# Performance work log

Hardware: AMD Instinct MI355X
Metric: run time of the kernel (lower is better)

## Reference

```python
import jax, jax.numpy as jnp
import numpy as np

B, N, E, C = 1, 100000, 1600000, 128


def setup_inputs() -> dict:
    key = jax.random.key(0)
    k1, k2, k3, k4 = jax.random.split(key, 4)
    x = jax.random.normal(k1, (B, N, C), dtype=jnp.float32)
    edge_index = jax.random.randint(k2, (2, E), 0, N, dtype=jnp.int32)
    W_2 = jax.random.normal(k3, (C,), dtype=jnp.float32)
    W_3 = jax.random.normal(k4, (C,), dtype=jnp.float32)
    return {"x": x, "edge_index": edge_index, "W_2": W_2, "W_3": W_3}


def reference(x, edge_index, W_2, W_3):
    # x: [B, N, C]; edge_index: [2, E] (src, dst)
    src, dst = edge_index[0], edge_index[1]
    num_nodes = x.shape[1]
    # per-edge attention weight: w[b,e] = <(x*W_3)[b,src_e], x[b,dst_e]>
    x3 = (x * W_3)[:, src, :]          # [B, E, C] gather
    x4 = x[:, dst, :]                  # [B, E, C] gather
    w = jnp.einsum('bec,bec->be', x3, x4)  # [B, E]
    # value messages with diagonal W_2 scaling, scattered to destination nodes.
    # Equivalent to out = einsum('bij,bih->bjh', dense_adj(w), x*W_2),
    # where dense_adj[src,dst] = w (to_dense_adj sums duplicate edges; so does segment_sum).
    x2 = x * W_2                       # [B, N, C]
    msg = w[..., None] * x2[:, src, :]  # [B, E, C]
    out = jax.vmap(lambda m: jax.ops.segment_sum(m, dst, num_segments=num_nodes))(msg)
    return out  # [B, N, C]
```

## Files before the change

### kernel.cpp

```cpp
#include <hip/hip_runtime.h>
#include <hip/hip_fp16.h>


#define CCH 128
#define BSHIFT 5
#define BWIDTH 32
#define MAXBIN 4096
#define CH 8192
#define LDSCAP 1280
#define TBINS 16
#define NBLKCAP 256


__global__ __launch_bounds__(256) void k_pack_hist(
    const float* __restrict__ x, __half* __restrict__ xh, int n4, int nPack,
    const int* __restrict__ dst, int E, int NBIN, int* __restrict__ hist_bm)
{
    __shared__ int cnt[MAXBIN];
    const int tid = threadIdx.x;

    if (blockIdx.x < nPack) {
        const int i = blockIdx.x * 256 + tid;
        if (i < n4) {
            float4 v = reinterpret_cast<const float4*>(x)[i];
            __half2* o = reinterpret_cast<__half2*>(xh) + (size_t)i * 2;
            o[0] = __floats2half2_rn(v.x, v.y);
            o[1] = __floats2half2_rn(v.z, v.w);
        }
        return;
    }

    const int blk = blockIdx.x - nPack;
    for (int b = tid; b < NBIN; b += 256) cnt[b] = 0;
    __syncthreads();

    const int e0 = blk * CH;
    #pragma unroll
    for (int k = 0; k < CH / 1024; ++k) {
        const int g = (e0 >> 2) + k * 256 + tid;
        const int e = g << 2;
        if (e >= E) continue;
        if (e + 4 <= E) {
            const int4 d4 = reinterpret_cast<const int4*>(dst)[g];
            atomicAdd(&cnt[d4.x >> BSHIFT], 1);
            atomicAdd(&cnt[d4.y >> BSHIFT], 1);
            atomicAdd(&cnt[d4.z >> BSHIFT], 1);
            atomicAdd(&cnt[d4.w >> BSHIFT], 1);
        } else {
            for (int ee = e; ee < E; ++ee) atomicAdd(&cnt[dst[ee] >> BSHIFT], 1);
        }
    }
    __syncthreads();
    int* hb = hist_bm + (size_t)blk * NBIN;
    for (int b = tid; b < NBIN; b += 256) hb[b] = cnt[b];
}


__global__ __launch_bounds__(256) void k_pscan(
    const int* __restrict__ hist_bm, int NBIN, int NBLK, int E_unused,
    int* __restrict__ scanned, unsigned int* __restrict__ status)
{
    __shared__ int tile[TBINS][NBLKCAP + 1];
    __shared__ int sdata[256];
    __shared__ int sbase;
    const int t = threadIdx.x;
    const int B0 = blockIdx.x * TBINS;

    for (int g = t; g < TBINS * (NBLKCAP + 1); g += 256)
        (&tile[0][0])[g] = 0;
    __syncthreads();

    for (int g = t; g < NBLK * TBINS; g += 256) {
        const int blk = g >> 4;
        const int tb  = g & (TBINS - 1);
        const int bin = B0 + tb;
        if (bin < NBIN) tile[tb][blk] = hist_bm[(size_t)blk * NBIN + bin];
    }
    __syncthreads();

    const int tb  = t >> 4;
    const int bk0 = (t & 15) * 16;
    int v[16];
    int local = 0;
    #pragma unroll
    for (int k = 0; k < 16; ++k) { v[k] = tile[tb][bk0 + k]; local += v[k]; }

    sdata[t] = local;
    __syncthreads();
    #pragma unroll
    for (int off = 1; off < 256; off <<= 1) {
        int val = (t >= off) ? sdata[t - off] : 0;
        __syncthreads();
        sdata[t] += val;
        __syncthreads();
    }
    const int incl = sdata[t];
    const int total = sdata[255];

    if (t == 0) {
        __hip_atomic_store(&status[blockIdx.x], (1u << 30) | (unsigned)total,
                           __ATOMIC_RELAXED, __HIP_MEMORY_SCOPE_AGENT);
        int base = 0;
        for (int j = (int)blockIdx.x - 1; j >= 0; --j) {
            unsigned w;
            do {
                w = __hip_atomic_load(&status[j], __ATOMIC_RELAXED,
                                      __HIP_MEMORY_SCOPE_AGENT);
            } while ((w >> 30) == 0u);
            base += (int)(w & 0x3FFFFFFFu);
            if ((w >> 30) == 2u) break;
        }
        __hip_atomic_store(&status[blockIdx.x],
                           (2u << 30) | (unsigned)(base + total),
                           __ATOMIC_RELAXED, __HIP_MEMORY_SCOPE_AGENT);
        sbase = base;
    }
    __syncthreads();

    int run = sbase + (incl - local);
    const int bin = B0 + tb;
    if (bin < NBIN) {
        #pragma unroll
        for (int k = 0; k < 16; ++k) {
            const int blk = bk0 + k;
            if (blk < NBLK) scanned[(size_t)bin * NBLK + blk] = run;
            run += v[k];
        }
    }
}


__global__ __launch_bounds__(256) void k_place(
    const int* __restrict__ src, const int* __restrict__ dst, int E, int NBIN, int NBLK,
    const int* __restrict__ scanned, unsigned int* __restrict__ coarse)
{
    __shared__ int lcur[MAXBIN];
    const int blk = blockIdx.x;
    const int tid = threadIdx.x;
    for (int b = tid; b < NBIN; b += 256)
        lcur[b] = scanned[(size_t)b * NBLK + blk];
    __syncthreads();

    const int e0 = blk * CH;
    #pragma unroll
    for (int k = 0; k < CH / 1024; ++k) {
        const int g = (e0 >> 2) + k * 256 + tid;
        const int e = g << 2;
        if (e >= E) continue;
        if (e + 4 <= E) {
            const int4 d4 = reinterpret_cast<const int4*>(dst)[g];
            const int4 s4 = reinterpret_cast<const int4*>(src)[g];
            int p;
            p = atomicAdd(&lcur[d4.x >> BSHIFT], 1);
            coarse[p] = (unsigned)s4.x | ((unsigned)(d4.x & (BWIDTH - 1)) << 17);
            p = atomicAdd(&lcur[d4.y >> BSHIFT], 1);
            coarse[p] = (unsigned)s4.y | ((unsigned)(d4.y & (BWIDTH - 1)) << 17);
            p = atomicAdd(&lcur[d4.z >> BSHIFT], 1);
            coarse[p] = (unsigned)s4.z | ((unsigned)(d4.z & (BWIDTH - 1)) << 17);
            p = atomicAdd(&lcur[d4.w >> BSHIFT], 1);
            coarse[p] = (unsigned)s4.w | ((unsigned)(d4.w & (BWIDTH - 1)) << 17);
        } else {
            for (int ee = e; ee < E; ++ee) {
                const int d = dst[ee], s = src[ee];
                int p = atomicAdd(&lcur[d >> BSHIFT], 1);
                coarse[p] = (unsigned)s | ((unsigned)(d & (BWIDTH - 1)) << 17);
            }
        }
    }
}


__global__ __launch_bounds__(256) void k_sort_accum(
    const __half* __restrict__ xh,
    const float* __restrict__ W2,
    const float* __restrict__ W3,
    const unsigned int* __restrict__ coarse,
    const int* __restrict__ scanned,
    int NBIN, int NBLK, int E, int N,
    float* __restrict__ out)
{
    __shared__ unsigned int raw[LDSCAP];
    __shared__ int srcl[LDSCAP];
    __shared__ int cnt[BWIDTH], offs[BWIDTH], cur[BWIDTH];

    const int bin  = blockIdx.x;
    const int tid  = threadIdx.x;
    const int lane = tid & 63;
    const int grp  = lane >> 4;
    const int sl   = lane & 15;
    const int gid  = (tid >> 6) * 4 + grp;
    const int choff = sl << 4;
    const char* xb = (const char*)xh;

    union H { int4 i4; __half2 h[4]; };

    const int node0 = (bin << BSHIFT) + gid * 2;
    const int node1 = node0 + 1;
    H uD0, uD1;
    uD0.i4 = make_int4(0, 0, 0, 0);
    uD1.i4 = make_int4(0, 0, 0, 0);
    if (node0 < N) uD0.i4 = *reinterpret_cast<const int4*>(xb + (((size_t)node0) << 8) + choff);
    if (node1 < N) uD1.i4 = *reinterpret_cast<const int4*>(xb + (((size_t)node1) << 8) + choff);

    const size_t i0 = (size_t)bin * NBLK;
    const int beg = scanned[i0];
    const int end = (bin + 1 < NBIN) ? scanned[i0 + NBLK] : E;
    const int mtot = end - beg;
    const int m = (mtot < LDSCAP) ? mtot : LDSCAP;

    if (tid < BWIDTH) cnt[tid] = 0;
    __syncthreads();

    for (int i = tid; i < m; i += 256) {
        unsigned u = coarse[beg + i];
        raw[i] = u;
        atomicAdd(&cnt[u >> 17], 1);
    }
    __syncthreads();

    if (tid < BWIDTH) {
        int c = cnt[tid];
        int v = c;
        #pragma unroll
        for (int d2 = 1; d2 < BWIDTH; d2 <<= 1) {
            int t2 = __shfl_up(v, d2, 64);
            if (tid >= d2) v += t2;
        }
        offs[tid] = v - c;
        cur[tid]  = v - c;
    }
    __syncthreads();

    for (int i = tid; i < m; i += 256) {
        const unsigned u = raw[i];
        const int p = atomicAdd(&cur[u >> 17], 1);
        srcl[p] = (int)(u & 0x1FFFFu);
    }
    __syncthreads();

    const float4 w3a = *reinterpret_cast<const float4*>(W3 + sl * 8);
    const float4 w3b = *reinterpret_cast<const float4*>(W3 + sl * 8 + 4);
    const float4 w2a = *reinterpret_cast<const float4*>(W2 + sl * 8);
    const float4 w2b = *reinterpret_cast<const float4*>(W2 + sl * 8 + 4);

    #pragma unroll
    for (int i = 0; i < 2; ++i) {
        const int node = (i == 0) ? node0 : node1;
        if (node >= N) continue;
        const int dl = gid * 2 + i;
        const H uD = (i == 0) ? uD0 : uD1;

        const float2 e0 = __half22float2(uD.h[0]);
        const float2 e1 = __half22float2(uD.h[1]);
        const float2 e2 = __half22float2(uD.h[2]);
        const float2 e3 = __half22float2(uD.h[3]);
        const float4 va = make_float4(w3a.x * e0.x, w3a.y * e0.y,
                                      w3a.z * e1.x, w3a.w * e1.y);
        const float4 vb = make_float4(w3b.x * e2.x, w3b.y * e2.y,
                                      w3b.z * e3.x, w3b.w * e3.y);

        float4 accA = make_float4(0.f, 0.f, 0.f, 0.f);
        float4 accB = make_float4(0.f, 0.f, 0.f, 0.f);

        const int b0 = offs[dl];
        const int c  = cnt[dl];

        int j = 0;
        for (; j + 4 <= c; j += 4) {
            const int s0 = srcl[b0 + j];
            const int s1 = srcl[b0 + j + 1];
            const int s2 = srcl[b0 + j + 2];
            const int s3 = srcl[b0 + j + 3];
            H u0, u1, u2, u3;
            u0.i4 = *reinterpret_cast<const int4*>(xb + (((size_t)s0) << 8) + choff);
            u1.i4 = *reinterpret_cast<const int4*>(xb + (((size_t)s1) << 8) + choff);
            u2.i4 = *reinterpret_cast<const int4*>(xb + (((size_t)s2) << 8) + choff);
            u3.i4 = *reinterpret_cast<const int4*>(xb + (((size_t)s3) << 8) + choff);
            const float2 f00 = __half22float2(u0.h[0]);
            const float2 f01 = __half22float2(u0.h[1]);
            const float2 f02 = __half22float2(u0.h[2]);
            const float2 f03 = __half22float2(u0.h[3]);
            const float2 f10 = __half22float2(u1.h[0]);
            const float2 f11 = __half22float2(u1.h[1]);
            const float2 f12 = __half22float2(u1.h[2]);
            const float2 f13 = __half22float2(u1.h[3]);
            const float2 f20 = __half22float2(u2.h[0]);
            const float2 f21 = __half22float2(u2.h[1]);
            const float2 f22 = __half22float2(u2.h[2]);
            const float2 f23 = __half22float2(u2.h[3]);
            const float2 f30 = __half22float2(u3.h[0]);
            const float2 f31 = __half22float2(u3.h[1]);
            const float2 f32 = __half22float2(u3.h[2]);
            const float2 f33 = __half22float2(u3.h[3]);
            float p0 = f00.x * va.x + f00.y * va.y + f01.x * va.z + f01.y * va.w
                     + f02.x * vb.x + f02.y * vb.y + f03.x * vb.z + f03.y * vb.w;
            float p1 = f10.x * va.x + f10.y * va.y + f11.x * va.z + f11.y * va.w
                     + f12.x * vb.x + f12.y * vb.y + f13.x * vb.z + f13.y * vb.w;
            float p2 = f20.x * va.x + f20.y * va.y + f21.x * va.z + f21.y * va.w
                     + f22.x * vb.x + f22.y * vb.y + f23.x * vb.z + f23.y * vb.w;
            float p3 = f30.x * va.x + f30.y * va.y + f31.x * va.z + f31.y * va.w
                     + f32.x * vb.x + f32.y * vb.y + f33.x * vb.z + f33.y * vb.w;
            #pragma unroll
            for (int off = 1; off < 16; off <<= 1) {
                p0 += __shfl_xor(p0, off, 64);
                p1 += __shfl_xor(p1, off, 64);
                p2 += __shfl_xor(p2, off, 64);
                p3 += __shfl_xor(p3, off, 64);
            }
            accA.x += p0 * f00.x + p1 * f10.x + p2 * f20.x + p3 * f30.x;
            accA.y += p0 * f00.y + p1 * f10.y + p2 * f20.y + p3 * f30.y;
            accA.z += p0 * f01.x + p1 * f11.x + p2 * f21.x + p3 * f31.x;
            accA.w += p0 * f01.y + p1 * f11.y + p2 * f21.y + p3 * f31.y;
            accB.x += p0 * f02.x + p1 * f12.x + p2 * f22.x + p3 * f32.x;
            accB.y += p0 * f02.y + p1 * f12.y + p2 * f22.y + p3 * f32.y;
            accB.z += p0 * f03.x + p1 * f13.x + p2 * f23.x + p3 * f33.x;
            accB.w += p0 * f03.y + p1 * f13.y + p2 * f23.y + p3 * f33.y;
        }
        for (; j < c; ++j) {
            H u0;
            u0.i4 = *reinterpret_cast<const int4*>(
                xb + (((size_t)srcl[b0 + j]) << 8) + choff);
            const float2 f0 = __half22float2(u0.h[0]);
            const float2 f1 = __half22float2(u0.h[1]);
            const float2 f2 = __half22float2(u0.h[2]);
            const float2 f3 = __half22float2(u0.h[3]);
            float p = f0.x * va.x + f0.y * va.y + f1.x * va.z + f1.y * va.w
                    + f2.x * vb.x + f2.y * vb.y + f3.x * vb.z + f3.y * vb.w;
            #pragma unroll
            for (int off = 1; off < 16; off <<= 1) p += __shfl_xor(p, off, 64);
            accA.x += p * f0.x; accA.y += p * f0.y;
            accA.z += p * f1.x; accA.w += p * f1.y;
            accB.x += p * f2.x; accB.y += p * f2.y;
            accB.z += p * f3.x; accB.w += p * f3.y;
        }
        for (int i2 = LDSCAP; i2 < mtot; ++i2) {
            const unsigned u = coarse[beg + i2];
            if ((int)(u >> 17) != dl) continue;
            H u0;
            u0.i4 = *reinterpret_cast<const int4*>(
                xb + (((size_t)(u & 0x1FFFFu)) << 8) + choff);
            const float2 f0 = __half22float2(u0.h[0]);
            const float2 f1 = __half22float2(u0.h[1]);
            const float2 f2 = __half22float2(u0.h[2]);
            const float2 f3 = __half22float2(u0.h[3]);
            float p = f0.x * va.x + f0.y * va.y + f1.x * va.z + f1.y * va.w
                    + f2.x * vb.x + f2.y * vb.y + f3.x * vb.z + f3.y * vb.w;
            #pragma unroll
            for (int off = 1; off < 16; off <<= 1) p += __shfl_xor(p, off, 64);
            accA.x += p * f0.x; accA.y += p * f0.y;
            accA.z += p * f1.x; accA.w += p * f1.y;
            accB.x += p * f2.x; accB.y += p * f2.y;
            accB.z += p * f3.x; accB.w += p * f3.y;
        }

        accA.x *= w2a.x; accA.y *= w2a.y; accA.z *= w2a.z; accA.w *= w2a.w;
        accB.x *= w2b.x; accB.y *= w2b.y; accB.z *= w2b.z; accB.w *= w2b.w;
        float* orow = out + (size_t)node * CCH + sl * 8;
        *reinterpret_cast<float4*>(orow)     = accA;
        *reinterpret_cast<float4*>(orow + 4) = accB;
    }
}


__global__ __launch_bounds__(256) void edge_gather_scatter(
    const float* __restrict__ x, const int* __restrict__ edge_index,
    const float* __restrict__ W2, const float* __restrict__ W3,
    float* __restrict__ out, int E)
{
    const int e    = (blockIdx.x * blockDim.x + threadIdx.x) >> 6;
    const int lane = threadIdx.x & 63;
    if (e >= E) return;
    const int s = edge_index[e];
    const int d = edge_index[E + e];
    const float2 xs = *reinterpret_cast<const float2*>(x + (size_t)s * CCH + lane * 2);
    const float2 xd = *reinterpret_cast<const float2*>(x + (size_t)d * CCH + lane * 2);
    const float2 w3 = *reinterpret_cast<const float2*>(W3 + lane * 2);
    const float2 w2 = *reinterpret_cast<const float2*>(W2 + lane * 2);
    float p = xs.x * w3.x * xd.x + xs.y * w3.y * xd.y;
    #pragma unroll
    for (int off = 32; off > 0; off >>= 1) p += __shfl_xor(p, off, 64);
    float* o = out + (size_t)d * CCH + lane * 2;
    atomicAdd(o,     p * xs.x * w2.x);
    atomicAdd(o + 1, p * xs.y * w2.y);
}


extern "C" void kernel_launch(void* const* d_in, const int* in_sizes, int n_in,
                              void* d_out, int out_size, void* d_ws, size_t ws_size,
                              hipStream_t stream) {
    const float* x          = (const float*)d_in[0];
    const int*   edge_index = (const int*)  d_in[1];
    const float* W2         = (const float*)d_in[2];
    const float* W3         = (const float*)d_in[3];
    float*       out        = (float*)d_out;

    const int E = in_sizes[1] / 2;
    const int N = out_size / CCH;
    const int* src = edge_index;
    const int* dst = edge_index + E;

    const int NBIN = (N + BWIDTH - 1) >> BSHIFT;
    const int NBLK = (E + CH - 1) / CH;
    const long long Mll = (long long)NBIN * NBLK;
    const int M = (int)Mll;
    const int nb1 = (NBIN + TBINS - 1) / TBINS;

    const size_t xh_bytes = (size_t)N * CCH * 2;
    const size_t need = xh_bytes + (size_t)E * 4 + 2 * (size_t)M * 4 + 4096;

    const bool aligned16 = (((uintptr_t)src & 15) == 0) && (((uintptr_t)dst & 15) == 0);

    if (N <= (1 << 17) && NBIN <= MAXBIN && NBLK <= NBLKCAP && Mll <= (1LL << 20) &&
        nb1 <= 1024 && aligned16 && ws_size >= need) {
        char* base = (char*)d_ws;
        __half* xh        = (__half*)base;       base += xh_bytes;
        unsigned* coarse  = (unsigned*)base;     base += (size_t)E * 4;
        int* hist_bm      = (int*)base;          base += (size_t)M * 4;
        int* scanned      = (int*)base;          base += (size_t)M * 4;
        unsigned* status  = (unsigned*)base;

        const int n4 = N * CCH / 4;
        const int nPack = (n4 + 255) / 256;

        hipMemsetAsync(status, 0, 1024 * sizeof(unsigned), stream);
        k_pack_hist<<<nPack + NBLK, 256, 0, stream>>>(x, xh, n4, nPack,
                                                      dst, E, NBIN, hist_bm);
        k_pscan<<<nb1, 256, 0, stream>>>(hist_bm, NBIN, NBLK, E, scanned, status);
        k_place<<<NBLK, 256, 0, stream>>>(src, dst, E, NBIN, NBLK, scanned, coarse);
        k_sort_accum<<<NBIN, 256, 0, stream>>>(xh, W2, W3, coarse, scanned,
                                               NBIN, NBLK, E, N, out);
        return;
    }

    hipMemsetAsync(d_out, 0, (size_t)out_size * sizeof(float), stream);
    const int grid = (E * 64 + 255) / 256;
    edge_gather_scatter<<<grid, 256, 0, stream>>>(x, edge_index, W2, W3, out, E);
}
```

Measured before the change: 139.3 us.

## Replace decoupled-lookback scan with two-pass scan and move fp16 pack into place kernel

The single-pass decoupled-lookback prefix scan, which needed a status memset and serial spinning, becomes a two-pass scan: per-tile partial sums, then a tiny single-block scan of the tile totals. Consumers now add the tile offset when they read. The x-to-fp16 pack moves from the histogram kernel into the placement kernel, so the short histogram pass runs alone and the pack overlaps with placement. This adds one kernel launch, removes the memset and the serial lookback chain, and adds an extra blocksum load per bin in consumers.

New measurement: 126.9 us. -8.9%, faster.

```diff
diff --git a/kernel.cpp b/kernel.cpp
--- a/kernel.cpp
+++ b/kernel.cpp
@@ -12,25 +12,12 @@
 #define NBLKCAP 256
 
 
-__global__ __launch_bounds__(256) void k_pack_hist(
-    const float* __restrict__ x, __half* __restrict__ xh, int n4, int nPack,
+__global__ __launch_bounds__(256) void k_hist(
     const int* __restrict__ dst, int E, int NBIN, int* __restrict__ hist_bm)
 {
     __shared__ int cnt[MAXBIN];
+    const int blk = blockIdx.x;
     const int tid = threadIdx.x;
-
-    if (blockIdx.x < nPack) {
-        const int i = blockIdx.x * 256 + tid;
-        if (i < n4) {
-            float4 v = reinterpret_cast<const float4*>(x)[i];
-            __half2* o = reinterpret_cast<__half2*>(xh) + (size_t)i * 2;
-            o[0] = __floats2half2_rn(v.x, v.y);
-            o[1] = __floats2half2_rn(v.z, v.w);
-        }
-        return;
-    }
-
-    const int blk = blockIdx.x - nPack;
     for (int b = tid; b < NBIN; b += 256) cnt[b] = 0;
     __syncthreads();
 
@@ -56,13 +43,12 @@
 }
 
 
-__global__ __launch_bounds__(256) void k_pscan(
-    const int* __restrict__ hist_bm, int NBIN, int NBLK, int E_unused,
-    int* __restrict__ scanned, unsigned int* __restrict__ status)
+__global__ __launch_bounds__(256) void k_pscan1(
+    const int* __restrict__ hist_bm, int NBIN, int NBLK,
+    int* __restrict__ partial, int* __restrict__ blocksum)
 {
     __shared__ int tile[TBINS][NBLKCAP + 1];
     __shared__ int sdata[256];
-    __shared__ int sbase;
     const int t = threadIdx.x;
     const int B0 = blockIdx.x * TBINS;
 
@@ -95,50 +81,61 @@
         __syncthreads();
     }
     const int incl = sdata[t];
-    const int total = sdata[255];
-
-    if (t == 0) {
-        __hip_atomic_store(&status[blockIdx.x], (1u << 30) | (unsigned)total,
-                           __ATOMIC_RELAXED, __HIP_MEMORY_SCOPE_AGENT);
-        int base = 0;
-        for (int j = (int)blockIdx.x - 1; j >= 0; --j) {
-            unsigned w;
-            do {
-                w = __hip_atomic_load(&status[j], __ATOMIC_RELAXED,
-                                      __HIP_MEMORY_SCOPE_AGENT);
-            } while ((w >> 30) == 0u);
-            base += (int)(w & 0x3FFFFFFFu);
-            if ((w >> 30) == 2u) break;
-        }
-        __hip_atomic_store(&status[blockIdx.x],
-                           (2u << 30) | (unsigned)(base + total),
-                           __ATOMIC_RELAXED, __HIP_MEMORY_SCOPE_AGENT);
-        sbase = base;
-    }
-    __syncthreads();
-
-    int run = sbase + (incl - local);
+    int run = incl - local;
+    if (t == 255) blocksum[blockIdx.x] = incl;
+
     const int bin = B0 + tb;
     if (bin < NBIN) {
         #pragma unroll
         for (int k = 0; k < 16; ++k) {
             const int blk = bk0 + k;
-            if (blk < NBLK) scanned[(size_t)bin * NBLK + blk] = run;
+            if (blk < NBLK) partial[(size_t)bin * NBLK + blk] = run;
             run += v[k];
         }
     }
 }
 
-
-__global__ __launch_bounds__(256) void k_place(
-    const int* __restrict__ src, const int* __restrict__ dst, int E, int NBIN, int NBLK,
-    const int* __restrict__ scanned, unsigned int* __restrict__ coarse)
+__global__ void k_scan2(int* __restrict__ blocksum, int nb) {
+    __shared__ int sdata[1024];
+    const int t = threadIdx.x;
+    const int v = (t < nb) ? blocksum[t] : 0;
+    sdata[t] = v;
+    __syncthreads();
+    for (int off = 1; off < 1024; off <<= 1) {
+        int val = (t >= off) ? sdata[t - off] : 0;
+        __syncthreads();
+        sdata[t] += val;
+        __syncthreads();
+    }
+    if (t < nb) blocksum[t] = sdata[t] - v;
+}
+
+
+__global__ __launch_bounds__(256) void k_pack_place(
+    const float* __restrict__ x, __half* __restrict__ xh, int n4,
+    const int* __restrict__ src, const int* __restrict__ dst, int E,
+    int NBIN, int NBLK,
+    const int* __restrict__ partial, const int* __restrict__ blocksum,
+    unsigned int* __restrict__ coarse)
 {
     __shared__ int lcur[MAXBIN];
+    const int tid = threadIdx.x;
+
+    if (blockIdx.x >= (unsigned)NBLK) {
+        const int i = (blockIdx.x - NBLK) * 256 + tid;
+        if (i < n4) {
+            float4 v = reinterpret_cast<const float4*>(x)[i];
+            __half2* o = reinterpret_cast<__half2*>(xh) + (size_t)i * 2;
+            o[0] = __floats2half2_rn(v.x, v.y);
+            o[1] = __floats2half2_rn(v.z, v.w);
+        }
+        return;
+    }
+
     const int blk = blockIdx.x;
-    const int tid = threadIdx.x;
-    for (int b = tid; b < NBIN; b += 256)
-        lcur[b] = scanned[(size_t)b * NBLK + blk];
+    for (int b = tid; b < NBIN; b += 256) {
+        lcur[b] = partial[(size_t)b * NBLK + blk] + blocksum[b / TBINS];
+    }
     __syncthreads();
 
     const int e0 = blk * CH;
@@ -175,7 +172,7 @@
     const float* __restrict__ W2,
     const float* __restrict__ W3,
     const unsigned int* __restrict__ coarse,
-    const int* __restrict__ scanned,
+    const int* __restrict__ partial, const int* __restrict__ blocksum,
     int NBIN, int NBLK, int E, int N,
     float* __restrict__ out)
 {
@@ -203,8 +200,9 @@
     if (node1 < N) uD1.i4 = *reinterpret_cast<const int4*>(xb + (((size_t)node1) << 8) + choff);
 
     const size_t i0 = (size_t)bin * NBLK;
-    const int beg = scanned[i0];
-    const int end = (bin + 1 < NBIN) ? scanned[i0 + NBLK] : E;
+    const int beg = partial[i0] + blocksum[bin / TBINS];
+    const int end = (bin + 1 < NBIN)
+        ? partial[i0 + NBLK] + blocksum[(bin + 1) / TBINS] : E;
     const int mtot = end - beg;
     const int m = (mtot < LDSCAP) ? mtot : LDSCAP;
 
@@ -406,28 +404,30 @@
     const int nb1 = (NBIN + TBINS - 1) / TBINS;
 
     const size_t xh_bytes = (size_t)N * CCH * 2;
-    const size_t need = xh_bytes + (size_t)E * 4 + 2 * (size_t)M * 4 + 4096;
+    const size_t need = xh_bytes + (size_t)E * 4 + 2 * (size_t)M * 4 + 1024 * 4;
 
     const bool aligned16 = (((uintptr_t)src & 15) == 0) && (((uintptr_t)dst & 15) == 0);
 
     if (N <= (1 << 17) && NBIN <= MAXBIN && NBLK <= NBLKCAP && Mll <= (1LL << 20) &&
         nb1 <= 1024 && aligned16 && ws_size >= need) {
         char* base = (char*)d_ws;
-        __half* xh        = (__half*)base;       base += xh_bytes;
-        unsigned* coarse  = (unsigned*)base;     base += (size_t)E * 4;
-        int* hist_bm      = (int*)base;          base += (size_t)M * 4;
-        int* scanned      = (int*)base;          base += (size_t)M * 4;
-        unsigned* status  = (unsigned*)base;
+        __half* xh       = (__half*)base;        base += xh_bytes;
+        unsigned* coarse = (unsigned*)base;      base += (size_t)E * 4;
+        int* hist_bm     = (int*)base;           base += (size_t)M * 4;
+        int* partial     = (int*)base;           base += (size_t)M * 4;
+        int* blocksum    = (int*)base;
 
         const int n4 = N * CCH / 4;
         const int nPack = (n4 + 255) / 256;
 
-        hipMemsetAsync(status, 0, 1024 * sizeof(unsigned), stream);
-        k_pack_hist<<<nPack + NBLK, 256, 0, stream>>>(x, xh, n4, nPack,
-                                                      dst, E, NBIN, hist_bm);
-        k_pscan<<<nb1, 256, 0, stream>>>(hist_bm, NBIN, NBLK, E, scanned, status);
-        k_place<<<NBLK, 256, 0, stream>>>(src, dst, E, NBIN, NBLK, scanned, coarse);
-        k_sort_accum<<<NBIN, 256, 0, stream>>>(xh, W2, W3, coarse, scanned,
+        k_hist<<<NBLK, 256, 0, stream>>>(dst, E, NBIN, hist_bm);
+        k_pscan1<<<nb1, 256, 0, stream>>>(hist_bm, NBIN, NBLK, partial, blocksum);
+        k_scan2<<<1, 1024, 0, stream>>>(blocksum, nb1);
+        k_pack_place<<<NBLK + nPack, 256, 0, stream>>>(x, xh, n4, src, dst, E,
+                                                       NBIN, NBLK,
+                                                       partial, blocksum, coarse);
+        k_sort_accum<<<NBIN, 256, 0, stream>>>(xh, W2, W3, coarse,
+                                               partial, blocksum,
                                                NBIN, NBLK, E, N, out);
         return;
     }
```
